# Kernel tuning notes

Measured on AMD Instinct MI355X. Metric: run time of the kernel, lower is better.

The kernel has to match this reference:

```python
import jax, jax.numpy as jnp
import numpy as np

B = 4; IMG = 32; P = 2; CIN = 3; G = IMG // P; N = G * G; D = 768; NL = 8
DI = 1536; NH = 24; HD = 64; DS = 128; CONVDIM = DI + 2 * DS; DPROJ = 2 * DI + 2 * DS + NH
OUTC = 3 * CIN; FREQ = 256; EPS = 1e-6


def _sincos_1d(dim, pos):
    omega = np.arange(dim // 2, dtype=np.float64) / (dim / 2.0)
    omega = 1.0 / 10000 ** omega
    out = np.einsum('m,d->md', pos.reshape(-1), omega)
    return np.concatenate([np.sin(out), np.cos(out)], axis=1)


def _pos_embed_2d(dim, gs):
    gh = np.arange(gs, dtype=np.float32)
    gw = np.arange(gs, dtype=np.float32)
    grid = np.stack(np.meshgrid(gw, gh), axis=0)
    return np.concatenate([_sincos_1d(dim // 2, grid[0]), _sincos_1d(dim // 2, grid[1])], axis=1)


POS = jnp.asarray(_pos_embed_2d(D, G), dtype=jnp.float32)[None]  # [1, N, D]


def _ln(x):
    m = x.mean(-1, keepdims=True)
    v = ((x - m) ** 2).mean(-1, keepdims=True)
    return (x - m) * jax.lax.rsqrt(v + EPS)


def _patch_embed(img, w, b):
    # conv with kernel=stride=P == reshape to (c, ph, pw)-ordered patch vectors + matmul
    xp = img.reshape(B, CIN, G, P, G, P).transpose(0, 2, 4, 1, 3, 5).reshape(B, N, CIN * P * P)
    return xp @ w + b


def _t_embed(t, tw1, tb1, tw2, tb2):
    half = FREQ // 2
    freqs = jnp.exp(-jnp.log(10000.0) * jnp.arange(half, dtype=jnp.float32) / half)
    args = t[:, None] * freqs[None]
    emb = jnp.concatenate([jnp.cos(args), jnp.sin(args)], axis=-1)
    return jax.nn.silu(emb @ tw1 + tb1) @ tw2 + tb2


def _mamba2(u, in_w, conv_w, conv_b, dt_bias, A_log, D_ssm, out_w):
    # u: [B, N, D]
    zxbcdt = u @ in_w                           # [B, N, DPROJ]
    z = zxbcdt[..., :DI]
    xBC = zxbcdt[..., DI:DI + CONVDIM]
    dt_raw = zxbcdt[..., DI + CONVDIM:]
    # causal depthwise conv1d, kernel 4
    pad = jnp.pad(xBC, ((0, 0), (3, 0), (0, 0)))
    xBC = sum(pad[:, k:k + N, :] * conv_w[:, k] for k in range(4)) + conv_b
    xBC = jax.nn.silu(xBC)
    xs = xBC[..., :DI].reshape(B, N, NH, HD)
    Bm = xBC[..., DI:DI + DS]
    Cm = xBC[..., DI + DS:]
    dt = jax.nn.softplus(dt_raw + dt_bias)       # [B, N, NH]
    a = dt * (-jnp.exp(A_log))                   # [B, N, NH], negative
    acum = jnp.cumsum(a, axis=1)
    seg = acum[:, :, None, :] - acum[:, None, :, :]   # [B, l, s, NH]
    tril = jnp.tril(jnp.ones((N, N), bool))
    decay = jnp.exp(jnp.where(tril[None, :, :, None], seg, -1e30))
    decay = jnp.moveaxis(decay, -1, 1)           # [B, NH, l, s]
    CB = jnp.einsum('bln,bsn->bls', Cm, Bm)
    scores = CB[:, None] * decay * jnp.moveaxis(dt, -1, 1)[:, :, None, :]
    y = jnp.einsum('bhls,bshp->blhp', scores, xs) + D_ssm[None, None, :, None] * xs
    y = y.reshape(B, N, DI) * jax.nn.silu(z)
    return y @ out_w


def _conv3(x, w, b):
    o = jax.lax.conv_general_dilated(x, w, (1, 1), 'SAME',
                                     dimension_numbers=('NCHW', 'OIHW', 'NCHW'))
    return o + b[None, :, None, None]


def _hfnet(h, w1, b1, w2, b2, w3, b3):
    c = jax.nn.relu(_conv3(h, w1, b1))
    c = jax.nn.relu(_conv3(c, w2, b2))
    return h + _conv3(c, w3, b3)


def _forward(x, t, y, H1, H2, H3, xe_w, xe_b, ye_w, ye_b, tw1, tb1, tw2, tb2,
             adaln_w, adaln_b, in_w, conv_w, conv_b, dt_bias, A_log, D_ssm, out_w,
             fl_t_w, fl_t_b, fl_y_w, fl_y_b, fl_lin_w, fl_lin_b,
             e1_w1, e1_b1, e1_w2, e1_b2, e1_w3, e1_b3,
             e2_w1, e2_b1, e2_w2, e2_b2, e2_w3, e2_b3,
             e3_w1, e3_b1, e3_w2, e3_b2, e3_w3, e3_b3):
    xe = _patch_embed(x, xe_w, xe_b) + POS
    ye = _patch_embed(y, ye_w, ye_b) + POS
    te = _t_embed(t, tw1, tb1, tw2, tb2)
    st = jax.nn.silu(te)          # [B, D]
    sy = jax.nn.silu(ye)          # [B, N, D]

    def layer(xc, p):
        aw, ab, iw, cw, cb, db, al, dd, ow = p
        sh_t, sc_t, g_t = jnp.split(st @ aw + ab, 3, axis=-1)
        sh_y, sc_y, g_y = jnp.split(sy @ aw + ab, 3, axis=-1)
        shift = sh_t[:, None] + sh_y
        scale = sc_t[:, None] + sc_y
        gate = g_t[:, None] + g_y
        xm = _ln(xc) * (1.0 + scale) + shift
        return gate * _mamba2(xm, iw, cw, cb, db, al, dd, ow) + xc, None

    xh, _ = jax.lax.scan(layer, xe, (adaln_w, adaln_b, in_w, conv_w, conv_b,
                                     dt_bias, A_log, D_ssm, out_w))
    sh_t, sc_t = jnp.split(st @ fl_t_w + fl_t_b, 2, axis=-1)
    sh_y, sc_y = jnp.split(sy @ fl_y_w + fl_y_b, 2, axis=-1)
    xf = (_ln(xh) * (1.0 + sc_t[:, None] + sc_y) + sh_t[:, None] + sh_y) @ fl_lin_w + fl_lin_b
    # unpatchify: nhwpqc -> nchpwq
    img = xf.reshape(B, G, G, P, P, OUTC).transpose(0, 5, 1, 3, 2, 4).reshape(B, OUTC, IMG, IMG)
    h1 = _hfnet(H1, e1_w1, e1_b1, e1_w2, e1_b2, e1_w3, e1_b3)
    h2 = _hfnet(H2, e2_w1, e2_b1, e2_w2, e2_b2, e2_w3, e2_b3)
    h3 = _hfnet(H3, e3_w1, e3_b1, e3_w2, e3_b2, e3_w3, e3_b3)
    return (img, h1, h2, h3)


def setup_inputs() -> dict:
    ks = iter(jax.random.split(jax.random.key(0), 80))
    def nrm(shape, s=0.02):
        return jax.random.normal(next(ks), shape, jnp.float32) * s
    z = lambda *s: jnp.zeros(s, jnp.float32)
    inp = {}
    inp['x'] = jax.random.normal(next(ks), (B, CIN, IMG, IMG), jnp.float32)
    inp['t'] = jax.random.uniform(next(ks), (B,), jnp.float32) * 1000.0
    inp['y'] = jax.random.normal(next(ks), (B, CIN, IMG, IMG), jnp.float32)
    inp['H1'] = jax.random.normal(next(ks), (B, CIN, IMG, IMG), jnp.float32)
    inp['H2'] = jax.random.normal(next(ks), (B, CIN, IMG, IMG), jnp.float32)
    inp['H3'] = jax.random.normal(next(ks), (B, CIN, IMG, IMG), jnp.float32)
    inp['xe_w'] = nrm((CIN * P * P, D), 0.1); inp['xe_b'] = z(D)
    inp['ye_w'] = nrm((CIN * P * P, D), 0.1); inp['ye_b'] = z(D)
    inp['tw1'] = nrm((FREQ, D)); inp['tb1'] = z(D)
    inp['tw2'] = nrm((D, D)); inp['tb2'] = z(D)
    inp['adaln_w'] = nrm((NL, D, 3 * D)); inp['adaln_b'] = nrm((NL, 3 * D))
    inp['in_w'] = nrm((NL, D, DPROJ))
    inp['conv_w'] = nrm((NL, CONVDIM, 4), 0.2); inp['conv_b'] = z(NL, CONVDIM)
    inp['dt_bias'] = nrm((NL, NH), 0.5)
    inp['A_log'] = jnp.tile(jnp.log(jnp.arange(1.0, NH + 1.0, dtype=jnp.float32)), (NL, 1))
    inp['D_ssm'] = jnp.ones((NL, NH), jnp.float32)
    inp['out_w'] = nrm((NL, DI, D))
    inp['fl_t_w'] = nrm((D, 2 * D)); inp['fl_t_b'] = z(2 * D)
    inp['fl_y_w'] = nrm((D, 2 * D)); inp['fl_y_b'] = z(2 * D)
    inp['fl_lin_w'] = nrm((D, P * P * OUTC)); inp['fl_lin_b'] = z(P * P * OUTC)
    for i in (1, 2, 3):
        inp['e%d_w1' % i] = nrm((64, CIN, 3, 3), 0.1); inp['e%d_b1' % i] = z(64)
        inp['e%d_w2' % i] = nrm((64, 64, 3, 3), 0.05); inp['e%d_b2' % i] = z(64)
        inp['e%d_w3' % i] = nrm((CIN, 64, 3, 3), 0.05); inp['e%d_b3' % i] = z(CIN)
    return inp


def reference(x, t, y, H1, H2, H3, xe_w, xe_b, ye_w, ye_b, tw1, tb1, tw2, tb2,
              adaln_w, adaln_b, in_w, conv_w, conv_b, dt_bias, A_log, D_ssm, out_w,
              fl_t_w, fl_t_b, fl_y_w, fl_y_b, fl_lin_w, fl_lin_b,
              e1_w1, e1_b1, e1_w2, e1_b2, e1_w3, e1_b3,
              e2_w1, e2_b1, e2_w2, e2_b2, e2_w3, e2_b3,
              e3_w1, e3_b1, e3_w2, e3_b2, e3_w3, e3_b3):
    return _forward(x, t, y, H1, H2, H3, xe_w, xe_b, ye_w, ye_b, tw1, tb1, tw2, tb2,
                    adaln_w, adaln_b, in_w, conv_w, conv_b, dt_bias, A_log, D_ssm, out_w,
                    fl_t_w, fl_t_b, fl_y_w, fl_y_b, fl_lin_w, fl_lin_b,
                    e1_w1, e1_b1, e1_w2, e1_b2, e1_w3, e1_b3,
                    e2_w1, e2_b1, e2_w2, e2_b2, e2_w3, e2_b3,
                    e3_w1, e3_b1, e3_w2, e3_b2, e3_w3, e3_b3)
```

## Files before the change

kernel.cpp:

```cpp
#include <hip/hip_runtime.h>
#include <cmath>

namespace {

constexpr int kB = 4;
constexpr int kN = 256;
constexpr int kD = 768;
constexpr int kNL = 8;
constexpr int kDI = 1536;
constexpr int kNH = 24;
constexpr int kHD = 64;
constexpr int kCONV = 1792;
constexpr int kDPROJ = 3352;
constexpr int kD3 = 2304;
constexpr int kNCAT = 19968;
constexpr int kOFF_FL = 18432;

typedef __attribute__((ext_vector_type(8))) short short8;
typedef __attribute__((ext_vector_type(4))) float f32x4;

__device__ __forceinline__ float siluf(float x) { return x / (1.f + expf(-x)); }

__device__ __forceinline__ short f2bf(float f) {
  unsigned u = __float_as_uint(f);
  unsigned r = (u + 0x7fffu + ((u >> 16) & 1u)) >> 16;
  return (short)r;
}

__device__ __forceinline__ void gload_lds16(const void* g, void* l) {
  __builtin_amdgcn_global_load_lds(
      (const __attribute__((address_space(1))) void*)g,
      (__attribute__((address_space(3))) void*)l, 16, 0, 0);
}

template <int N> __device__ __forceinline__ void wait_barrier();
template <> __device__ __forceinline__ void wait_barrier<0>() {
  asm volatile("s_waitcnt vmcnt(0)\n\ts_barrier" ::: "memory");
}
template <> __device__ __forceinline__ void wait_barrier<2>() {
  asm volatile("s_waitcnt vmcnt(2)\n\ts_barrier" ::: "memory");
}
template <> __device__ __forceinline__ void wait_barrier<3>() {
  asm volatile("s_waitcnt vmcnt(3)\n\ts_barrier" ::: "memory");
}
template <> __device__ __forceinline__ void wait_barrier<4>() {
  asm volatile("s_waitcnt vmcnt(4)\n\ts_barrier" ::: "memory");
}

__global__ void patch_embed2_kernel(const float* __restrict__ img0,
                                    const float* __restrict__ w0,
                                    const float* __restrict__ b0,
                                    float* __restrict__ out0,
                                    const float* __restrict__ img1,
                                    const float* __restrict__ w1,
                                    const float* __restrict__ b1,
                                    float* __restrict__ out1,
                                    short* __restrict__ out1_bf) {
  int gid = blockIdx.x * blockDim.x + threadIdx.x;
  if (gid >= kB * kN * kD) return;
  int z = blockIdx.z;
  const float* img = z ? img1 : img0;
  const float* w = z ? w1 : w0;
  const float* bias = z ? b1 : b0;
  int d = gid % kD;
  int n = (gid / kD) % kN;
  int b = gid / (kD * kN);
  int gi = n >> 4, gj = n & 15;
  float acc = bias[d];
#pragma unroll
  for (int c = 0; c < 3; ++c)
#pragma unroll
    for (int pi = 0; pi < 2; ++pi)
#pragma unroll
      for (int pj = 0; pj < 2; ++pj) {
        float v = img[((b * 3 + c) * 32 + gi * 2 + pi) * 32 + gj * 2 + pj];
        acc += v * w[(c * 4 + pi * 2 + pj) * kD + d];
      }
  float pos;
  if (d < 192)       pos = sinf((float)gj * powf(10000.f, -(float)d / 192.f));
  else if (d < 384)  pos = cosf((float)gj * powf(10000.f, -(float)(d - 192) / 192.f));
  else if (d < 576)  pos = sinf((float)gi * powf(10000.f, -(float)(d - 384) / 192.f));
  else               pos = cosf((float)gi * powf(10000.f, -(float)(d - 576) / 192.f));
  acc += pos;
  if (z) {
    float v = siluf(acc);
    out1[gid] = v;
    out1_bf[gid] = f2bf(v);
  } else {
    out0[gid] = acc;
  }
}

__global__ void tembed_args_kernel(const float* __restrict__ t,
                                   float* __restrict__ ctst) {
  int idx = blockIdx.x * 256 + threadIdx.x;
  if (idx >= kB * 256) return;
  int b = idx >> 8, j = idx & 255;
  int k = j & 127;
  float f = expf(-9.210340371976184f * (float)k / 128.f);
  float arg = t[b] * f;
  ctst[idx] = (j < 128) ? cosf(arg) : sinf(arg);
}

__global__ __launch_bounds__(256) void splitk_mm_stage1(
    const float* __restrict__ A, const float* __restrict__ W,
    float* __restrict__ part, int K, int Nn, int KC) {
  int n = blockIdx.x * 256 + threadIdx.x;
  int kc = blockIdx.y;
  int l = blockIdx.z;
  if (n >= Nn) return;
  const float* w = W + (size_t)l * K * Nn + (size_t)kc * 64 * Nn + n;
  int kb = kc * 64;
  float a0 = 0.f, a1 = 0.f, a2 = 0.f, a3 = 0.f;
  for (int k = 0; k < 64; ++k) {
    float wv = w[(size_t)k * Nn];
    a0 += A[0 * K + kb + k] * wv;
    a1 += A[1 * K + kb + k] * wv;
    a2 += A[2 * K + kb + k] * wv;
    a3 += A[3 * K + kb + k] * wv;
  }
  size_t base = (((size_t)l * KC + kc) * 4) * Nn + n;
  part[base] = a0;
  part[base + Nn] = a1;
  part[base + 2 * (size_t)Nn] = a2;
  part[base + 3 * (size_t)Nn] = a3;
}

__global__ void splitk_mm_reduce(const float* __restrict__ part,
                                 const float* __restrict__ bias,
                                 float* __restrict__ C, int Nn, int KC, int L,
                                 int act) {
  int idx = blockIdx.x * 256 + threadIdx.x;
  if (idx >= L * 4 * Nn) return;
  int n = idx % Nn;
  int b = (idx / Nn) & 3;
  int l = idx / (4 * Nn);
  float s = bias[(size_t)l * Nn + n];
  for (int kc = 0; kc < KC; ++kc)
    s += part[(((size_t)l * KC + kc) * 4 + b) * Nn + n];
  C[idx] = act ? siluf(s) : s;
}

__global__ __launch_bounds__(256) void transposeW_kernel(
    const float* __restrict__ W, short* __restrict__ Wt, int K, int N,
    size_t sW, size_t sWt) {
  W += (size_t)blockIdx.z * sW;
  Wt += (size_t)blockIdx.z * sWt;
  __shared__ float tile[32][33];
  int n0 = blockIdx.x * 32, k0 = blockIdx.y * 32;
  int tid = threadIdx.x;
  int tx = tid & 31, ty = tid >> 5;
#pragma unroll
  for (int i = 0; i < 4; ++i) {
    int k = k0 + ty + i * 8;
    int n = n0 + tx;
    tile[ty + i * 8][tx] = (n < N) ? W[(size_t)k * N + n] : 0.f;
  }
  __syncthreads();
#pragma unroll
  for (int i = 0; i < 4; ++i) {
    int n = n0 + ty + i * 8;
    int k = k0 + tx;
    Wt[(size_t)n * K + k] = f2bf(tile[tx][ty + i * 8]);
  }
}

__global__ void concat_bias_kernel(const float* __restrict__ a,
                                   const float* __restrict__ b,
                                   float* __restrict__ dst) {
  int i = blockIdx.x * 256 + threadIdx.x;
  if (i < kOFF_FL) dst[i] = a[i];
  else if (i < kNCAT) dst[i] = b[i - kOFF_FL];
}

template <int BM, int BN>
__global__ __launch_bounds__(256) void mfma_gemm(
    const short* __restrict__ A, const short* __restrict__ Bt,
    const float* __restrict__ bias, float* __restrict__ C,
    int Nn, int Ksplit, int Ktot, int ldc, size_t czstride) {
  constexpr int MI = BM / 32;
  constexpr int NJ = BN / 32;
  constexpr int LPW = BM / 64 + BN / 64;
  __shared__ short Als[3 * BM * 32];
  __shared__ short Bls[3 * BN * 32];
  int gx = gridDim.x, gy = gridDim.y;
  int nblk = gx * gy;
  int hl = blockIdx.y * gx + blockIdx.x;
  int txi, tyi;
  if ((nblk & 7) == 0) {
    int chunk = nblk >> 3;
    int s_id = (hl & 7) * chunk + (hl >> 3);
    txi = s_id / gy;
    tyi = s_id % gy;
  } else {
    txi = blockIdx.x;
    tyi = blockIdx.y;
  }
  int m0 = tyi * BM, n0 = txi * BN;
  int koff = blockIdx.z * Ksplit;
  C += (size_t)blockIdx.z * czstride;
  int tid = threadIdx.x;
  int lane = tid & 63, wid = tid >> 6;
  int wr = wid >> 1, wc = wid & 1;
  f32x4 acc[MI][NJ] = {};
  int sm = tid >> 2;
  int sk = (tid & 3) * 8;
  const int nsteps = Ksplit >> 5;
  auto stage = [&](int buf, int k0) {
#pragma unroll
    for (int h = 0; h < BM / 64; ++h)
      gload_lds16(&A[(size_t)(m0 + h * 64 + sm) * Ktot + koff + k0 + sk],
                  &Als[buf * (BM * 32) + h * 2048 + wid * 512]);
#pragma unroll
    for (int h = 0; h < BN / 64; ++h)
      gload_lds16(&Bt[(size_t)(n0 + h * 64 + sm) * Ktot + koff + k0 + sk],
                  &Bls[buf * (BN * 32) + h * 2048 + wid * 512]);
  };
  stage(0, 0);
  if (nsteps > 1) stage(1, 32);
  int cur = 0;
  for (int s = 0; s < nsteps; ++s) {
    if (s + 1 < nsteps) wait_barrier<LPW>();
    else wait_barrier<0>();
    if (s + 2 < nsteps) stage(cur == 0 ? 2 : cur - 1, (s + 2) << 5);
    short8 av[MI], bv[NJ];
#pragma unroll
    for (int mi = 0; mi < MI; ++mi)
      av[mi] = *(const short8*)&Als[cur * (BM * 32) +
                                    (wr * (BM / 2) + mi * 16 + (lane & 15)) *
                                        32 +
                                    (lane >> 4) * 8];
#pragma unroll
    for (int nj = 0; nj < NJ; ++nj)
      bv[nj] = *(const short8*)&Bls[cur * (BN * 32) +
                                    (wc * (BN / 2) + nj * 16 + (lane & 15)) *
                                        32 +
                                    (lane >> 4) * 8];
#pragma unroll
    for (int mi = 0; mi < MI; ++mi)
#pragma unroll
      for (int nj = 0; nj < NJ; ++nj)
        acc[mi][nj] = __builtin_amdgcn_mfma_f32_16x16x32_bf16(
            av[mi], bv[nj], acc[mi][nj], 0, 0, 0);
    cur = (cur == 2) ? 0 : cur + 1;
  }
#pragma unroll
  for (int mi = 0; mi < MI; ++mi)
#pragma unroll
    for (int nj = 0; nj < NJ; ++nj)
#pragma unroll
      for (int r = 0; r < 4; ++r) {
        int gm = m0 + wr * (BM / 2) + mi * 16 + (lane >> 4) * 4 + r;
        int gn = n0 + wc * (BN / 2) + nj * 16 + (lane & 15);
        if (gn >= Nn) continue;
        C[(size_t)gm * ldc + gn] = acc[mi][nj][r] + (bias ? bias[gn] : 0.f);
      }
}

__global__ __launch_bounds__(256) void ln_mod_kernel(
    const float* __restrict__ x, const float* __restrict__ tA,
    const float* __restrict__ yA, short* __restrict__ out_bf, int tstride,
    int ystride, const float* __restrict__ p0, const float* __restrict__ p1,
    const float* __restrict__ gtA, const float* __restrict__ gyA,
    float* __restrict__ xcw) {
  int row = blockIdx.x;
  int b = row >> 8;
  int tid = threadIdx.x;
  __shared__ float w1[4], w2[4];
  float xr[3];
  float s = 0.f;
#pragma unroll
  for (int k = 0; k < 3; ++k) {
    int i = tid + k * 256;
    float v = x[(size_t)row * kD + i];
    if (p0) {
      float g = gtA[b * kD3 + 2 * kD + i] +
                gyA[(size_t)row * kNCAT + 2 * kD + i];
      v += g * (p0[(size_t)row * kD + i] + p1[(size_t)row * kD + i]);
      xcw[(size_t)row * kD + i] = v;
    }
    xr[k] = v;
    s += v;
  }
#pragma unroll
  for (int o = 32; o > 0; o >>= 1) s += __shfl_down(s, o, 64);
  if ((tid & 63) == 0) w1[tid >> 6] = s;
  __syncthreads();
  float mean = (w1[0] + w1[1] + w1[2] + w1[3]) * (1.f / kD);
  float s2 = 0.f;
#pragma unroll
  for (int k = 0; k < 3; ++k) {
    float d = xr[k] - mean;
    s2 += d * d;
  }
#pragma unroll
  for (int o = 32; o > 0; o >>= 1) s2 += __shfl_down(s2, o, 64);
  if ((tid & 63) == 0) w2[tid >> 6] = s2;
  __syncthreads();
  float rstd = rsqrtf((w2[0] + w2[1] + w2[2] + w2[3]) * (1.f / kD) + 1e-6f);
#pragma unroll
  for (int k = 0; k < 3; ++k) {
    int i = tid + k * 256;
    float sc = tA[b * tstride + kD + i] + yA[(size_t)row * ystride + kD + i];
    float sh = tA[b * tstride + i] + yA[(size_t)row * ystride + i];
    float v = (xr[k] - mean) * rstd * (1.f + sc) + sh;
    out_bf[(size_t)row * kD + i] = f2bf(v);
  }
}

__global__ __launch_bounds__(256) void convdt_kernel(
    const float* __restrict__ zx, const float* __restrict__ cw,
    const float* __restrict__ cb, const float* __restrict__ db,
    const float* __restrict__ al, float* __restrict__ xbc,
    short* __restrict__ bB, short* __restrict__ bC, float* __restrict__ dts,
    float* __restrict__ acum) {
  constexpr int kConvBlocks = kB * kN * kCONV / 256;
  int blk = blockIdx.x;
  if (blk < kConvBlocks) {
    int idx = blk * 256 + threadIdx.x;
    int c = idx % kCONV;
    int row = idx / kCONV;
    int n = row & 255, b = row >> 8;
    float acc = cb[c];
#pragma unroll
    for (int k = 0; k < 4; ++k) {
      int ns = n + k - 3;
      if (ns >= 0)
        acc += zx[(size_t)(b * kN + ns) * kDPROJ + kDI + c] * cw[c * 4 + k];
    }
    float v = siluf(acc);
    xbc[idx] = v;
    if (c >= kDI) {
      if (c < kDI + 128)
        bB[(size_t)row * 128 + (c - kDI)] = f2bf(v);
      else
        bC[(size_t)row * 128 + (c - kDI - 128)] = f2bf(v);
    }
  } else {
    int bh = blk - kConvBlocks;
    int b = bh / kNH, h = bh % kNH;
    int n = threadIdx.x;
    __shared__ float sb[256];
    size_t row = (size_t)(b * kN + n);
    float xv = zx[row * kDPROJ + (kDI + kCONV) + h] + db[h];
    float dt = xv > 20.f ? xv : log1pf(expf(xv));
    dts[row * kNH + h] = dt;
    float a = -expf(al[h]) * dt;
    sb[n] = a;
    __syncthreads();
    for (int off = 1; off < 256; off <<= 1) {
      float v = (n >= off) ? sb[n - off] : 0.f;
      __syncthreads();
      sb[n] += v;
      __syncthreads();
    }
    acum[row * kNH + h] = sb[n];
  }
}

__global__ __launch_bounds__(256) void ssm_y_kernel(
    const short* __restrict__ bCm, const short* __restrict__ bBm,
    const float* __restrict__ acum, const float* __restrict__ dts,
    const float* __restrict__ xbc, const float* __restrict__ zx,
    const float* __restrict__ Dssm, short* __restrict__ ybuf) {
  int bh = blockIdx.z;
  int b = bh / kNH, h = bh % kNH;
  int m0 = blockIdx.y * 64;
  int tid = threadIdx.x;
  int lane = tid & 63, wid = tid >> 6;
  int tx = tid & 15, ty = tid >> 4;
  __shared__ float As[16][65];
  __shared__ float Xs[16][64];
  float acc[4][4] = {};
  float acum_l[4];
#pragma unroll
  for (int r = 0; r < 4; ++r) {
    int l = m0 + wid * 16 + (lane >> 4) * 4 + r;
    acum_l[r] = acum[(size_t)(b * kN + l) * kNH + h];
  }
  const short* cRow =
      &bCm[((size_t)(b * kN + m0 + wid * 16 + (lane & 15))) * 128 +
           (lane >> 4) * 8];
  for (int k0 = 0; k0 < kN; k0 += 16) {
    if (k0 > m0 + 63) break;
    f32x4 cb = {};
    const short* bRow =
        &bBm[((size_t)(b * kN + k0 + (lane & 15))) * 128 + (lane >> 4) * 8];
#pragma unroll
    for (int ks = 0; ks < 4; ++ks)
      cb = __builtin_amdgcn_mfma_f32_16x16x32_bf16(
          *(const short8*)(cRow + ks * 32), *(const short8*)(bRow + ks * 32),
          cb, 0, 0, 0);
    int ss = k0 + (lane & 15);
    float acum_ss = acum[(size_t)(b * kN + ss) * kNH + h];
    float dts_ss = dts[(size_t)(b * kN + ss) * kNH + h];
#pragma unroll
    for (int i = 0; i < 4; ++i) {
      int e = tid + i * 256;
      int k = e >> 6, n = e & 63;
      Xs[k][n] = xbc[(size_t)(b * kN + k0 + k) * kCONV + h * kHD + n];
    }
#pragma unroll
    for (int r = 0; r < 4; ++r) {
      int mloc = wid * 16 + (lane >> 4) * 4 + r;
      int l = m0 + mloc;
      float v = 0.f;
      if (ss <= l) v = cb[r] * expf(acum_l[r] - acum_ss) * dts_ss;
      As[lane & 15][mloc] = v;
    }
    __syncthreads();
#pragma unroll
    for (int kk = 0; kk < 16; ++kk) {
      float a[4], bb[4];
#pragma unroll
      for (int i = 0; i < 4; ++i) a[i] = As[kk][ty * 4 + i];
#pragma unroll
      for (int j = 0; j < 4; ++j) bb[j] = Xs[kk][tx * 4 + j];
#pragma unroll
      for (int i = 0; i < 4; ++i)
#pragma unroll
        for (int j = 0; j < 4; ++j) acc[i][j] += a[i] * bb[j];
    }
    __syncthreads();
  }
  float dd = Dssm[h];
#pragma unroll
  for (int i = 0; i < 4; ++i) {
    int l = m0 + ty * 4 + i;
    size_t row = (size_t)(b * kN + l);
#pragma unroll
    for (int j = 0; j < 4; ++j) {
      int p = tx * 4 + j;
      int col = h * kHD + p;
      float xs_l = xbc[row * kCONV + col];
      float yv = acc[i][j] + dd * xs_l;
      float zv = zx[row * kDPROJ + col];
      ybuf[row * kDI + col] = f2bf(yv * siluf(zv));
    }
  }
}

__global__ void unpatchify_kernel(const float* __restrict__ fpp,
                                  const float* __restrict__ bias,
                                  float* __restrict__ out) {
  constexpr int kFP = kB * kN * 36;
  int gid = blockIdx.x * 256 + threadIdx.x;
  if (gid >= kFP) return;
  int j = gid % 36;
  int row = gid / 36;
  int n = row & 255, b = row >> 8;
  int o = j % 9;
  int pj = (j / 9) & 1;
  int pi = j / 18;
  int gi = n >> 4, gj = n & 15;
  float v = fpp[gid] + fpp[kFP + gid] + fpp[2 * kFP + gid] +
            fpp[3 * kFP + gid] + bias[j];
  out[((b * 9 + o) * 32 + gi * 2 + pi) * 32 + (gj * 2 + pj)] = v;
}

__global__ __launch_bounds__(256) void conv1_kernel(
    const float* __restrict__ Ha, const float* __restrict__ Hb,
    const float* __restrict__ Hc, const float* __restrict__ wa,
    const float* __restrict__ wb, const float* __restrict__ wc,
    const float* __restrict__ ba, const float* __restrict__ bb,
    const float* __restrict__ bc, short* __restrict__ dst) {
  int gid = blockIdx.x * 256 + threadIdx.x;
  if (gid >= 3 * 4096 * 64) return;
  int oc = gid & 63;
  int px = (gid >> 6) & 4095;
  int net = gid >> 18;
  const float* in = net == 0 ? Ha : (net == 1 ? Hb : Hc);
  const float* w = net == 0 ? wa : (net == 1 ? wb : wc);
  const float* bs = net == 0 ? ba : (net == 1 ? bb : bc);
  int xx = px & 31, yy = (px >> 5) & 31, b = px >> 10;
  float acc = bs[oc];
#pragma unroll
  for (int ic = 0; ic < 3; ++ic) {
    const float* ip = in + ((size_t)(b * 3 + ic) << 10);
    const float* wp = w + (oc * 3 + ic) * 9;
#pragma unroll
    for (int ky = 0; ky < 3; ++ky) {
      int ys = yy + ky - 1;
      if (ys < 0 || ys > 31) continue;
#pragma unroll
      for (int kx = 0; kx < 3; ++kx) {
        int xs = xx + kx - 1;
        if (xs < 0 || xs > 31) continue;
        acc += ip[ys * 32 + xs] * wp[ky * 3 + kx];
      }
    }
  }
  dst[gid] = f2bf(fmaxf(acc, 0.f));
}

__global__ __launch_bounds__(256) void convw_prep_kernel(
    const float* __restrict__ w2a, const float* __restrict__ w2b,
    const float* __restrict__ w2c, const float* __restrict__ w3a,
    const float* __restrict__ w3b, const float* __restrict__ w3c,
    short* __restrict__ dst2, short* __restrict__ dst3) {
  int idx = blockIdx.x * 256 + threadIdx.x;
  if (idx >= 3 * 128 * 576) return;
  int z = blockIdx.z;
  int OC = z ? 3 : 64;
  short* dst = z ? dst3 : dst2;
  int k = idx % 576;
  int row = (idx / 576) & 127;
  int net = idx / (128 * 576);
  const float* w = z ? (net == 0 ? w3a : (net == 1 ? w3b : w3c))
                     : (net == 0 ? w2a : (net == 1 ? w2b : w2c));
  int pos = k >> 6, ic = k & 63;
  float v = (row < OC) ? w[row * 576 + ic * 9 + pos] : 0.f;
  dst[idx] = f2bf(v);
}

template <int EP>
__global__ __launch_bounds__(256) void conv_gemm(
    const short* __restrict__ src, const short* __restrict__ Btall,
    const float* __restrict__ b_a, const float* __restrict__ b_b,
    const float* __restrict__ b_c, const float* __restrict__ r_a,
    const float* __restrict__ r_b, const float* __restrict__ r_c,
    short* __restrict__ dst, float* __restrict__ outp) {
  constexpr int K = 576;
  __shared__ short Als[128 * 32];
  __shared__ short Bls[128 * 32];
  int net = blockIdx.z;
  int m0 = blockIdx.y * 128;
  const float* bias = net == 0 ? b_a : (net == 1 ? b_b : b_c);
  const float* res = net == 0 ? r_a : (net == 1 ? r_b : r_c);
  const short* Bt = Btall + (size_t)net * 128 * K;
  int tid = threadIdx.x;
  int lane = tid & 63, wid = tid >> 6;
  int wr = wid >> 1, wc = wid & 1;
  f32x4 acc[4][4] = {};
  int sm = tid >> 2;
  int sk = (tid & 3) * 8;
  for (int k0 = 0; k0 < K; k0 += 32) {
    int kk = k0 + sk;
    int pos = kk >> 6, ic0 = kk & 63;
    int ky = pos / 3 - 1, kx = pos % 3 - 1;
    uint4 a_st[2], b_st[2];
#pragma unroll
    for (int i = 0; i < 2; ++i) {
      int px = m0 + i * 64 + sm;
      int b = px >> 10;
      int yy = (px >> 5) & 31, xx = px & 31;
      int ys = yy + ky, xs = xx + kx;
      if (ys >= 0 && ys < 32 && xs >= 0 && xs < 32) {
        a_st[i] = *(const uint4*)&src[((size_t)(net * 4096 + (b << 10) +
                                                (ys << 5) + xs)
                                       << 6) +
                                      ic0];
      } else {
        a_st[i] = make_uint4(0u, 0u, 0u, 0u);
      }
      b_st[i] = *(const uint4*)&Bt[(size_t)(i * 64 + sm) * K + kk];
    }
    __syncthreads();
    *(uint4*)&Als[sm * 32 + sk] = a_st[0];
    *(uint4*)&Als[(64 + sm) * 32 + sk] = a_st[1];
    *(uint4*)&Bls[sm * 32 + sk] = b_st[0];
    *(uint4*)&Bls[(64 + sm) * 32 + sk] = b_st[1];
    __syncthreads();
    short8 av[4], bv[4];
#pragma unroll
    for (int mi = 0; mi < 4; ++mi)
      av[mi] = *(const short8*)&Als[(wr * 64 + mi * 16 + (lane & 15)) * 32 +
                                    (lane >> 4) * 8];
#pragma unroll
    for (int nj = 0; nj < 4; ++nj)
      bv[nj] = *(const short8*)&Bls[(wc * 64 + nj * 16 + (lane & 15)) * 32 +
                                    (lane >> 4) * 8];
#pragma unroll
    for (int mi = 0; mi < 4; ++mi)
#pragma unroll
      for (int nj = 0; nj < 4; ++nj)
        acc[mi][nj] = __builtin_amdgcn_mfma_f32_16x16x32_bf16(
            av[mi], bv[nj], acc[mi][nj], 0, 0, 0);
  }
#pragma unroll
  for (int mi = 0; mi < 4; ++mi)
#pragma unroll
    for (int nj = 0; nj < 4; ++nj)
#pragma unroll
      for (int r = 0; r < 4; ++r) {
        int gm = m0 + wr * 64 + mi * 16 + (lane >> 4) * 4 + r;
        int gn = wc * 64 + nj * 16 + (lane & 15);
        float v = acc[mi][nj][r];
        if (EP == 0) {
          if (gn < 64)
            dst[(size_t)(net * 4096 + gm) * 64 + gn] =
                f2bf(fmaxf(v + bias[gn], 0.f));
        } else {
          if (gn < 3) {
            int b = gm >> 10, pix = gm & 1023;
            size_t o = (size_t)(b * 3 + gn) * 1024 + pix;
            outp[36864 + net * 12288 + o] = v + bias[gn] + res[o];
          }
        }
      }
}

}

extern "C" void kernel_launch(void* const* d_in, const int* in_sizes, int n_in,
                              void* d_out, int out_size, void* d_ws,
                              size_t ws_size, hipStream_t stream) {
  const float* x = (const float*)d_in[0];
  const float* t = (const float*)d_in[1];
  const float* y = (const float*)d_in[2];
  const float* H[3] = {(const float*)d_in[3], (const float*)d_in[4],
                       (const float*)d_in[5]};
  const float* xe_w = (const float*)d_in[6];
  const float* xe_b = (const float*)d_in[7];
  const float* ye_w = (const float*)d_in[8];
  const float* ye_b = (const float*)d_in[9];
  const float* tw1 = (const float*)d_in[10];
  const float* tb1 = (const float*)d_in[11];
  const float* tw2 = (const float*)d_in[12];
  const float* tb2 = (const float*)d_in[13];
  const float* adaln_w = (const float*)d_in[14];
  const float* adaln_b = (const float*)d_in[15];
  const float* in_w = (const float*)d_in[16];
  const float* conv_w = (const float*)d_in[17];
  const float* conv_b = (const float*)d_in[18];
  const float* dt_bias = (const float*)d_in[19];
  const float* A_log = (const float*)d_in[20];
  const float* D_ssm = (const float*)d_in[21];
  const float* out_w = (const float*)d_in[22];
  const float* fl_t_w = (const float*)d_in[23];
  const float* fl_t_b = (const float*)d_in[24];
  const float* fl_y_w = (const float*)d_in[25];
  const float* fl_y_b = (const float*)d_in[26];
  const float* fl_lin_w = (const float*)d_in[27];
  const float* fl_lin_b = (const float*)d_in[28];

  float* out = (float*)d_out;
  float* ws = (float*)d_ws;

  size_t off = 0;
  auto alloc = [&](size_t nelem) { float* p = ws + off; off += nelem; return p; };
  float* xc    = alloc((size_t)kB * kN * kD);
  float* sy    = alloc((size_t)kB * kN * kD);
  short* sy_bf = (short*)alloc((size_t)kB * kN * kD / 2);
  float* st    = alloc((size_t)kB * kD);
  float* ht    = alloc((size_t)kB * kD);
  float* ctst  = alloc((size_t)kB * 256);
  float* tAall = alloc((size_t)kNL * kB * kD3);
  float* yA8   = alloc((size_t)kB * kN * kNCAT);
  short* xm_bf = (short*)alloc((size_t)kB * kN * kD / 2);
  float* zx    = alloc((size_t)kB * kN * kDPROJ);
  float* xbc   = alloc((size_t)kB * kN * kCONV);
  float* dts   = alloc((size_t)kB * kN * kNH);
  float* acum  = alloc((size_t)kB * kN * kNH);
  short* ybuf  = (short*)alloc((size_t)kB * kN * kDI / 2);
  float* tfl   = alloc((size_t)kB * 2 * kD);
  float* opart = alloc((size_t)2 * kB * kN * kD);
  float* fpp   = alloc((size_t)4 * kB * kN * 36);
  short* adalnT = (short*)alloc((size_t)kNCAT * kD / 2);
  float* biascat = alloc(kNCAT);
  short* in_wT = (short*)alloc((size_t)kNL * 3456 * kD / 2);
  short* Wt    = (short*)alloc((size_t)128 * kD / 2);
  short* bBm   = (short*)alloc((size_t)kB * kN * 128 / 2);
  short* bCm   = (short*)alloc((size_t)kB * kN * 128 / 2);
  short* c1bf  = (short*)alloc((size_t)3 * 4096 * 64 / 2);
  short* c2bf  = (short*)alloc((size_t)3 * 4096 * 64 / 2);
  short* Bt2   = (short*)alloc((size_t)3 * 128 * 576 / 2);
  short* Bt3   = (short*)alloc((size_t)3 * 128 * 576 / 2);
  (void)ws_size;

  float* part = zx;
  short* out_wT = adalnT;

  dim3 blk(256);

  patch_embed2_kernel<<<dim3((kB * kN * kD + 255) / 256, 1, 2), blk, 0,
                        stream>>>(x, xe_w, xe_b, xc, y, ye_w, ye_b, sy, sy_bf);

  transposeW_kernel<<<dim3(72, 24, kNL), blk, 0, stream>>>(
      adaln_w, adalnT, kD, kD3, (size_t)kD * kD3, (size_t)kD3 * kD);
  transposeW_kernel<<<dim3(48, 24, 1), blk, 0, stream>>>(
      fl_y_w, adalnT + (size_t)kOFF_FL * kD, kD, 2 * kD, 0, 0);
  concat_bias_kernel<<<dim3((kNCAT + 255) / 256), blk, 0, stream>>>(
      adaln_b, fl_y_b, biascat);
  mfma_gemm<128, 128><<<dim3(kNCAT / 128, 8), blk, 0, stream>>>(
      sy_bf, adalnT, biascat, yA8, kNCAT, kD, kD, kNCAT, 0);

  transposeW_kernel<<<dim3(108, 24, kNL), blk, 0, stream>>>(
      in_w, in_wT, kD, kDPROJ, (size_t)kD * kDPROJ, (size_t)3456 * kD);
  transposeW_kernel<<<dim3(24, 48, kNL), blk, 0, stream>>>(
      out_w, out_wT, kDI, kD, (size_t)kDI * kD, (size_t)768 * kDI);

  tembed_args_kernel<<<dim3(4), blk, 0, stream>>>(t, ctst);
  splitk_mm_stage1<<<dim3(3, 4, 1), blk, 0, stream>>>(ctst, tw1, part, 256,
                                                      kD, 4);
  splitk_mm_reduce<<<dim3((kB * kD + 255) / 256), blk, 0, stream>>>(
      part, tb1, ht, kD, 4, 1, 1);
  splitk_mm_stage1<<<dim3(3, 12, 1), blk, 0, stream>>>(ht, tw2, part, kD, kD, 12);
  splitk_mm_reduce<<<dim3((kB * kD + 255) / 256), blk, 0, stream>>>(
      part, tb2, st, kD, 12, 1, 1);
  splitk_mm_stage1<<<dim3(9, 12, kNL), blk, 0, stream>>>(st, adaln_w, part, kD,
                                                         kD3, 12);
  splitk_mm_reduce<<<dim3((kNL * kB * kD3 + 255) / 256), blk, 0, stream>>>(
      part, adaln_b, tAall, kD3, 12, kNL, 0);
  splitk_mm_stage1<<<dim3(6, 12, 1), blk, 0, stream>>>(st, fl_t_w, part, kD,
                                                       2 * kD, 12);
  splitk_mm_reduce<<<dim3((kB * 2 * kD + 255) / 256), blk, 0, stream>>>(
      part, fl_t_b, tfl, 2 * kD, 12, 1, 0);

  for (int l = 0; l < kNL; ++l) {
    const float* cw = conv_w + (size_t)l * kCONV * 4;
    const float* cb = conv_b + (size_t)l * kCONV;
    const float* db = dt_bias + (size_t)l * kNH;
    const float* al = A_log + (size_t)l * kNH;
    const float* dd = D_ssm + (size_t)l * kNH;
    float* tA = tAall + (size_t)l * kB * kD3;
    const float* yAl = yA8 + (size_t)l * kD3;
    const float* ptA = l ? tAall + (size_t)(l - 1) * kB * kD3 : nullptr;
    const float* pyA = l ? yA8 + (size_t)(l - 1) * kD3 : nullptr;

    ln_mod_kernel<<<dim3(kB * kN), blk, 0, stream>>>(
        xc, tA, yAl, xm_bf, kD3, kNCAT, l ? opart : nullptr,
        l ? opart + (size_t)kB * kN * kD : nullptr, ptA, pyA, xc);
    mfma_gemm<64, 64><<<dim3(54, 16), blk, 0, stream>>>(
        xm_bf, in_wT + (size_t)l * 3456 * kD, nullptr, zx, kDPROJ, kD, kD,
        kDPROJ, 0);
    convdt_kernel<<<dim3(kB * kN * kCONV / 256 + kB * kNH), blk, 0, stream>>>(
        zx, cw, cb, db, al, xbc, bBm, bCm, dts, acum);
    ssm_y_kernel<<<dim3(1, kN / 64, kB * kNH), blk, 0, stream>>>(
        bCm, bBm, acum, dts, xbc, zx, dd, ybuf);
    mfma_gemm<64, 64><<<dim3(12, 16, 2), blk, 0, stream>>>(
        ybuf, out_wT + (size_t)l * 768 * kDI, nullptr, opart, kD, kD, kDI,
        kD, (size_t)kB * kN * kD);
  }

  ln_mod_kernel<<<dim3(kB * kN), blk, 0, stream>>>(
      xc, tfl, yA8 + kOFF_FL, xm_bf, 2 * kD, kNCAT, opart,
      opart + (size_t)kB * kN * kD, tAall + (size_t)7 * kB * kD3,
      yA8 + (size_t)7 * kD3, xc);
  transposeW_kernel<<<dim3(4, 24, 1), blk, 0, stream>>>(fl_lin_w, Wt, kD, 36,
                                                        0, 0);
  mfma_gemm<64, 128><<<dim3(1, 16, 4), blk, 0, stream>>>(
      xm_bf, Wt, nullptr, fpp, 36, 192, kD, 36, (size_t)kB * kN * 36);
  unpatchify_kernel<<<dim3((kB * kN * 36 + 255) / 256), blk, 0, stream>>>(
      fpp, fl_lin_b, out);

  const float* w1s[3] = {(const float*)d_in[29], (const float*)d_in[35],
                         (const float*)d_in[41]};
  const float* b1s[3] = {(const float*)d_in[30], (const float*)d_in[36],
                         (const float*)d_in[42]};
  const float* w2s[3] = {(const float*)d_in[31], (const float*)d_in[37],
                         (const float*)d_in[43]};
  const float* b2s[3] = {(const float*)d_in[32], (const float*)d_in[38],
                         (const float*)d_in[44]};
  const float* w3s[3] = {(const float*)d_in[33], (const float*)d_in[39],
                         (const float*)d_in[45]};
  const float* b3s[3] = {(const float*)d_in[34], (const float*)d_in[40],
                         (const float*)d_in[46]};
  convw_prep_kernel<<<dim3((3 * 128 * 576 + 255) / 256, 1, 2), blk, 0,
                      stream>>>(w2s[0], w2s[1], w2s[2], w3s[0], w3s[1],
                                w3s[2], Bt2, Bt3);
  conv1_kernel<<<dim3(3 * 4096 * 64 / 256), blk, 0, stream>>>(
      H[0], H[1], H[2], w1s[0], w1s[1], w1s[2], b1s[0], b1s[1], b1s[2], c1bf);
  conv_gemm<0><<<dim3(1, 32, 3), blk, 0, stream>>>(
      c1bf, Bt2, b2s[0], b2s[1], b2s[2], nullptr, nullptr, nullptr, c2bf,
      nullptr);
  conv_gemm<1><<<dim3(1, 32, 3), blk, 0, stream>>>(
      c2bf, Bt3, b3s[0], b3s[1], b3s[2], H[0], H[1], H[2], nullptr, out);
}
```

Measured before the change: 1.031 ms.

## Load GEMM B operand directly from global into registers, bypassing LDS

The B (weight) tile is no longer staged through shared memory. Each lane now loads its MFMA B fragment straight from global memory into registers, software-pipelined one K-step ahead, while A keeps the triple-buffered LDS path. The vmcnt waits are recomputed to count the extra outstanding register loads. This saves LDS capacity and LDS read traffic, but B rows are now re-read by both wave rows (no sharing across waves) and uses 64B-strided per-lane global loads that coalesce less well, and the vmcnt accounting relies on the compiler keeping the issue order it assumes.

```diff
diff --git a/kernel.cpp b/kernel.cpp
--- a/kernel.cpp
+++ b/kernel.cpp
@@ -33,6 +33,10 @@
       (__attribute__((address_space(3))) void*)l, 16, 0, 0);
 }
 
+__device__ __forceinline__ void order_fence() {
+  asm volatile("" ::: "memory");
+}
+
 template <int N> __device__ __forceinline__ void wait_barrier();
 template <> __device__ __forceinline__ void wait_barrier<0>() {
   asm volatile("s_waitcnt vmcnt(0)\n\ts_barrier" ::: "memory");
@@ -45,6 +49,12 @@
 }
 template <> __device__ __forceinline__ void wait_barrier<4>() {
   asm volatile("s_waitcnt vmcnt(4)\n\ts_barrier" ::: "memory");
+}
+template <> __device__ __forceinline__ void wait_barrier<5>() {
+  asm volatile("s_waitcnt vmcnt(5)\n\ts_barrier" ::: "memory");
+}
+template <> __device__ __forceinline__ void wait_barrier<6>() {
+  asm volatile("s_waitcnt vmcnt(6)\n\ts_barrier" ::: "memory");
 }
 
 __global__ void patch_embed2_kernel(const float* __restrict__ img0,
@@ -180,9 +190,8 @@
     int Nn, int Ksplit, int Ktot, int ldc, size_t czstride) {
   constexpr int MI = BM / 32;
   constexpr int NJ = BN / 32;
-  constexpr int LPW = BM / 64 + BN / 64;
+  constexpr int LA = BM / 64;
   __shared__ short Als[3 * BM * 32];
-  __shared__ short Bls[3 * BN * 32];
   int gx = gridDim.x, gy = gridDim.y;
   int nblk = gx * gy;
   int hl = blockIdx.y * gx + blockIdx.x;
@@ -206,24 +215,35 @@
   int sm = tid >> 2;
   int sk = (tid & 3) * 8;
   const int nsteps = Ksplit >> 5;
-  auto stage = [&](int buf, int k0) {
-#pragma unroll
-    for (int h = 0; h < BM / 64; ++h)
+  auto stageA = [&](int buf, int k0) {
+#pragma unroll
+    for (int h = 0; h < LA; ++h)
       gload_lds16(&A[(size_t)(m0 + h * 64 + sm) * Ktot + koff + k0 + sk],
                   &Als[buf * (BM * 32) + h * 2048 + wid * 512]);
-#pragma unroll
-    for (int h = 0; h < BN / 64; ++h)
-      gload_lds16(&Bt[(size_t)(n0 + h * 64 + sm) * Ktot + koff + k0 + sk],
-                  &Bls[buf * (BN * 32) + h * 2048 + wid * 512]);
   };
-  stage(0, 0);
-  if (nsteps > 1) stage(1, 32);
+  const short* bptr[NJ];
+#pragma unroll
+  for (int nj = 0; nj < NJ; ++nj)
+    bptr[nj] = &Bt[(size_t)(n0 + wc * (BN / 2) + nj * 16 + (lane & 15)) *
+                       Ktot +
+                   koff + (lane >> 4) * 8];
+  short8 bv_cur[NJ], bv_nxt[NJ];
+  stageA(0, 0);
+  if (nsteps > 1) stageA(1, 32);
+  order_fence();
+#pragma unroll
+  for (int nj = 0; nj < NJ; ++nj) bv_cur[nj] = *(const short8*)bptr[nj];
   int cur = 0;
   for (int s = 0; s < nsteps; ++s) {
-    if (s + 1 < nsteps) wait_barrier<LPW>();
-    else wait_barrier<0>();
-    if (s + 2 < nsteps) stage(cur == 0 ? 2 : cur - 1, (s + 2) << 5);
-    short8 av[MI], bv[NJ];
+    if (s + 1 < nsteps) wait_barrier<LA + NJ>();
+    else wait_barrier<NJ>();
+    if (s + 2 < nsteps) stageA(cur == 0 ? 2 : cur - 1, (s + 2) << 5);
+    if (s + 1 < nsteps) {
+#pragma unroll
+      for (int nj = 0; nj < NJ; ++nj)
+        bv_nxt[nj] = *(const short8*)(bptr[nj] + (s + 1) * 32);
+    }
+    short8 av[MI];
 #pragma unroll
     for (int mi = 0; mi < MI; ++mi)
       av[mi] = *(const short8*)&Als[cur * (BM * 32) +
@@ -231,17 +251,13 @@
                                         32 +
                                     (lane >> 4) * 8];
 #pragma unroll
-    for (int nj = 0; nj < NJ; ++nj)
-      bv[nj] = *(const short8*)&Bls[cur * (BN * 32) +
-                                    (wc * (BN / 2) + nj * 16 + (lane & 15)) *
-                                        32 +
-                                    (lane >> 4) * 8];
-#pragma unroll
     for (int mi = 0; mi < MI; ++mi)
 #pragma unroll
       for (int nj = 0; nj < NJ; ++nj)
         acc[mi][nj] = __builtin_amdgcn_mfma_f32_16x16x32_bf16(
-            av[mi], bv[nj], acc[mi][nj], 0, 0, 0);
+            av[mi], bv_cur[nj], acc[mi][nj], 0, 0, 0);
+#pragma unroll
+    for (int nj = 0; nj < NJ; ++nj) bv_cur[nj] = bv_nxt[nj];
     cur = (cur == 2) ? 0 : cur + 1;
   }
 #pragma unroll
```

Result: slower. 1.179 ms (+14.3%).
